# Kernel tuning notes

Hardware: AMD Instinct MI355X
Metric: run time of the kernel (lower is better)

The kernel has to match this reference:

```python
import jax, jax.numpy as jnp
import numpy as np

N, D, F, K = 50000, 256, 256, 10


def setup_inputs() -> dict:
    key = jax.random.key(0)
    k1, k2, k3, k4, k5, k6 = jax.random.split(key, 6)
    # neighbor indices in [-1, N); -1 marks padding (masked out in forward)
    return {
        "Z1": jax.random.normal(k1, (N, D), dtype=jnp.float32),
        "Z2": jax.random.normal(k2, (N, D), dtype=jnp.float32),
        "Wr": jax.random.normal(k3, (D, F), dtype=jnp.float32),
        "Wnr": jax.random.normal(k4, (D, F), dtype=jnp.float32),
        "n1": jax.random.randint(k5, (N, K), -1, N, dtype=jnp.int64),
        "n2": jax.random.randint(k6, (N, K), -1, N, dtype=jnp.int64),
    }


def _protein(Z, nb, Wr, Wnr):
    residues_signal = Z @ Wr                      # [N, F]
    neighbors_base_signal = Z @ Wnr               # [N, F]
    mask = (nb > -1)                              # [N, K]
    # index -1 wraps to last row (as in torch), then is zeroed by the mask
    feats = neighbors_base_signal[nb] * mask[..., None].astype(Z.dtype)  # [N, K, F]
    norm = jnp.maximum(mask.sum(axis=1), 1).astype(Z.dtype)[:, None]     # [N, 1]
    neighbors_signal = feats.sum(axis=1) / norm
    return jax.nn.relu(residues_signal + neighbors_signal)


def reference(Z1, Z2, Wr, Wnr, n1, n2):
    out1 = _protein(Z1, n1, Wr, Wnr)
    out2 = _protein(Z2, n2, Wr, Wnr)
    return jnp.stack([out1, out2])  # [2, N, F]
```

## Files before the change

kernel.cpp:

```cpp
#include <hip/hip_runtime.h>
#include <hip/hip_bf16.h>
#include <hip/hip_fp8.h>

#define NNODE 50000
#define MTOT  100000
#define NF    256
#define KNB   10

typedef unsigned short u16;
typedef float f32x4 __attribute__((ext_vector_type(4)));
typedef float f32x2 __attribute__((ext_vector_type(2)));
typedef short bf16x8 __attribute__((ext_vector_type(8)));

__device__ __forceinline__ u16 f2bf(float f) {
    unsigned u = __builtin_bit_cast(unsigned, f);
    unsigned r = (u + 0x7fffu + ((u >> 16) & 1u)) >> 16;
    return (u16)r;
}
__device__ __forceinline__ unsigned char f2f8(float f) {
    return (unsigned char)__hip_fp8_e4m3(f).__x;
}
__device__ __forceinline__ float f8tof(unsigned char b) {
    __hip_fp8_e4m3 h;
    h.__x = (__hip_fp8_storage_t)b;
    return (float)h;
}
template <int WORD>
__device__ __forceinline__ f32x2 cvt2_fp8(unsigned v) {
#if __has_builtin(__builtin_amdgcn_cvt_pk_f32_fp8)
    auto c = __builtin_amdgcn_cvt_pk_f32_fp8((int)v, WORD);
    f32x2 r; r.x = c[0]; r.y = c[1];
    return r;
#else
    unsigned s = WORD ? (v >> 16) : v;
    f32x2 r;
    r.x = f8tof((unsigned char)(s & 0xff));
    r.y = f8tof((unsigned char)((s >> 8) & 0xff));
    return r;
#endif
}
template <int WORD>
__device__ __forceinline__ unsigned pk_fp8(float a, float b, unsigned old) {
#if __has_builtin(__builtin_amdgcn_cvt_pk_fp8_f32)
    return (unsigned)__builtin_amdgcn_cvt_pk_fp8_f32(a, b, (int)old, WORD);
#else
    unsigned lo = (unsigned)f2f8(a) | ((unsigned)f2f8(b) << 8);
    return WORD ? ((old & 0x0000ffffu) | (lo << 16)) : ((old & 0xffff0000u) | lo);
#endif
}
__device__ __forceinline__ void gload_lds16(const void* g, void* l) {
    __builtin_amdgcn_global_load_lds(
        (const __attribute__((address_space(1))) unsigned int*)g,
        (__attribute__((address_space(3))) unsigned int*)l, 16, 0, 0);
}

__global__ __launch_bounds__(256) void cast_all(const float* __restrict__ Z1,
                                                const float* __restrict__ Z2,
                                                const float* __restrict__ Wr,
                                                const float* __restrict__ Wnr,
                                                u16* __restrict__ Zleft,
                                                unsigned char* __restrict__ Z8,
                                                u16* __restrict__ WT,
                                                unsigned char* __restrict__ WT8) {
    int b = blockIdx.x;
    if (b < 12500) {
        unsigned id = b * 256 + threadIdx.x;
        int m = id >> 5;
        int d = (id & 31) << 3;
        const float* src = (m < NNODE) ? (Z1 + (size_t)m * 256 + d)
                                       : (Z2 + (size_t)(m - NNODE) * 256 + d);
        float4 a = *(const float4*)src;
        float4 bb = *(const float4*)(src + 4);
        uint4 o;
        o.x = (unsigned)f2bf(a.x) | ((unsigned)f2bf(a.y) << 16);
        o.y = (unsigned)f2bf(a.z) | ((unsigned)f2bf(a.w) << 16);
        o.z = (unsigned)f2bf(bb.x) | ((unsigned)f2bf(bb.y) << 16);
        o.w = (unsigned)f2bf(bb.z) | ((unsigned)f2bf(bb.w) << 16);
        *(uint4*)(Zleft + (size_t)m * 256 + d) = o;
        uint2 o8;
        o8.x = (unsigned)f2f8(a.x) | ((unsigned)f2f8(a.y) << 8) |
               ((unsigned)f2f8(a.z) << 16) | ((unsigned)f2f8(a.w) << 24);
        o8.y = (unsigned)f2f8(bb.x) | ((unsigned)f2f8(bb.y) << 8) |
               ((unsigned)f2f8(bb.z) << 16) | ((unsigned)f2f8(bb.w) << 24);
        *(uint2*)(Z8 + (size_t)m * 256 + d) = o8;
    } else if (b < 12756) {
        int id = (b - 12500) * 256 + threadIdx.x;
        int n = id >> 8, k = id & 255;
        WT[n * 256 + k] = f2bf(Wr[(size_t)k * 256 + n]);
    } else {
        int id = (b - 12756) * 256 + threadIdx.x;
        int n = id >> 8, k = id & 255;
        WT8[n * 256 + k] = f2f8(Wnr[(size_t)k * 256 + n]);
    }
}

__device__ __forceinline__ void stageA(const u16* __restrict__ A, u16* dst,
                                       int m0, int kt, int t) {
    int row = t >> 2, gd = t & 3;
    int gs = gd ^ (row & 3);
    int grow = m0 + row;
    if (grow >= MTOT) grow = MTOT - 1;
    gload_lds16(A + (size_t)grow * 256 + kt + gs * 8, dst + t * 8);
}
__device__ __forceinline__ void stageBl(const u16* __restrict__ WT, u16* dst,
                                        int kt, int t) {
    #pragma unroll
    for (int rp = 0; rp < 2; ++rp) {
        int c = rp * 512 + t;
        int col = c >> 2, gd = c & 3;
        int gs = gd ^ (col & 3);
        gload_lds16(WT + (size_t)col * 256 + kt + gs * 8, dst + c * 8);
    }
}
__device__ __forceinline__ void stageBr(const unsigned char* __restrict__ WT8,
                                        unsigned char* dst, int ktr, int t) {
    #pragma unroll
    for (int rp = 0; rp < 2; ++rp) {
        int c = rp * 512 + t;
        int col = c >> 2, gd = c & 3;
        int gs = gd ^ (col & 3);
        gload_lds16(WT8 + (size_t)col * 256 + ktr + gs * 16, dst + c * 16);
    }
}

__device__ __forceinline__ void mfma_left(const u16* sAc, const u16* sBc, int lane,
                                          int wr, int wc, f32x4 (&acc)[4][4]) {
    const int hi = lane >> 4, l15 = lane & 15;
    bf16x8 af[4], bfr[4];
    #pragma unroll
    for (int i = 0; i < 4; ++i) {
        int row = wr * 64 + i * 16 + l15;
        af[i] = *(const bf16x8*)&sAc[row * 32 + ((hi ^ (row & 3)) << 3)];
    }
    #pragma unroll
    for (int j = 0; j < 4; ++j) {
        int col = wc * 64 + j * 16 + l15;
        bfr[j] = *(const bf16x8*)&sBc[col * 32 + ((hi ^ (col & 3)) << 3)];
    }
    #pragma unroll
    for (int i = 0; i < 4; ++i)
        #pragma unroll
        for (int j = 0; j < 4; ++j)
            acc[i][j] = __builtin_amdgcn_mfma_f32_16x16x32_bf16(af[i], bfr[j], acc[i][j], 0, 0, 0);
}
__device__ __forceinline__ void mfma_right(const unsigned char* sZc, const unsigned char* sBc,
                                           int ktr, int lane, int wr, int wc,
                                           f32x4 (&acc)[4][4]) {
    const int hi = lane >> 4, l15 = lane & 15;
    #pragma unroll
    for (int kk = 0; kk < 64; kk += 32) {
        long long az[4], bz[4];
        #pragma unroll
        for (int i = 0; i < 4; ++i) {
            int row = wr * 64 + i * 16 + l15;
            int gr = ((ktr + kk) >> 3) + hi;
            az[i] = *(const long long*)&sZc[row * 256 + ((gr ^ (row & 7)) << 3)];
        }
        #pragma unroll
        for (int j = 0; j < 4; ++j) {
            int col = wc * 64 + j * 16 + l15;
            int kb = kk + hi * 8;
            bz[j] = *(const long long*)&sBc[col * 64 + (((kb >> 4) ^ (col & 3)) << 4) + (kb & 15)];
        }
        #pragma unroll
        for (int i = 0; i < 4; ++i)
            #pragma unroll
            for (int j = 0; j < 4; ++j)
                acc[i][j] = __builtin_amdgcn_mfma_f32_16x16x32_fp8_fp8(az[i], bz[j], acc[i][j], 0, 0, 0);
    }
}

template <int S>
__device__ __forceinline__ void left_step(const u16* __restrict__ Zl,
                                          const u16* __restrict__ WT,
                                          const unsigned char* __restrict__ WT8,
                                          const unsigned char* __restrict__ Z8,
                                          const int* __restrict__ n1,
                                          const int* __restrict__ n2,
                                          u16* sA0, u16* sA1, u16* sB0, u16* sB1,
                                          unsigned char* sZ,
                                          int m0, int t, int lane, int w, int wr, int wc,
                                          f32x4 (&acc)[4][4]) {
    u16* sAcur = (S & 1) ? sA1 : sA0;
    u16* sAnxt = (S & 1) ? sA0 : sA1;
    u16* sBcur = (S & 1) ? sB1 : sB0;
    u16* sBnxt = (S & 1) ? sB0 : sB1;
    int rl = (w << 4) + (S << 1) + (lane >> 5);
    int g = m0 + rl;
    if (g >= MTOT) g = MTOT - 1;
    int p = (g >= NNODE);
    const int* nb = (p ? n2 : n1) + (size_t)(g - p * NNODE) * KNB;
    int idxa[KNB];
    #pragma unroll
    for (int q = 0; q < 5; ++q) {
        int2 v = *(const int2*)(nb + 2 * q);
        idxa[2 * q] = v.x;
        idxa[2 * q + 1] = v.y;
    }
    const unsigned char* zb = Z8 + (size_t)p * ((size_t)NNODE * 256) + ((lane & 31) << 3);
    uint2 gv[KNB];
    #pragma unroll
    for (int k = 0; k < KNB; ++k)
        gv[k] = *(const uint2*)(zb + (size_t)(idxa[k] > -1 ? idxa[k] : 0) * 256);
    if (S < 7) {
        stageA(Zl, sAnxt, m0, (S + 1) * 32, t);
        stageBl(WT, sBnxt, (S + 1) * 32, t);
    } else {
        stageBr(WT8, (unsigned char*)sBnxt, 0, t);
    }
    f32x2 a0 = {0.f, 0.f}, a1 = {0.f, 0.f}, a2 = {0.f, 0.f}, a3 = {0.f, 0.f};
    int cnt = 0;
    #pragma unroll
    for (int k = 0; k < KNB; ++k) {
        int valid = (idxa[k] > -1) ? 1 : 0;
        cnt += valid;
        float mm = (float)valid;
        f32x2 m2 = {mm, mm};
        uint2 v = gv[k];
        a0 += m2 * cvt2_fp8<0>(v.x);
        a1 += m2 * cvt2_fp8<1>(v.x);
        a2 += m2 * cvt2_fp8<0>(v.y);
        a3 += m2 * cvt2_fp8<1>(v.y);
    }
    float sc = 1.0f / (float)(cnt > 0 ? cnt : 1);
    unsigned w0 = pk_fp8<0>(a0.x * sc, a0.y * sc, 0u);
    w0 = pk_fp8<1>(a1.x * sc, a1.y * sc, w0);
    unsigned w1 = pk_fp8<0>(a2.x * sc, a2.y * sc, 0u);
    w1 = pk_fp8<1>(a3.x * sc, a3.y * sc, w1);
    int gp = (lane & 31) ^ (rl & 7);
    *(uint2*)(sZ + rl * 256 + (gp << 3)) = make_uint2(w0, w1);
    if (S == 7) asm volatile("s_waitcnt lgkmcnt(0)" ::: "memory");
    __builtin_amdgcn_s_barrier();
    __builtin_amdgcn_s_setprio(1);
    mfma_left(sAcur, sBcur, lane, wr, wc, acc);
    __builtin_amdgcn_s_setprio(0);
    __builtin_amdgcn_s_barrier();
}

template <int R>
__device__ __forceinline__ void right_step(const unsigned char* __restrict__ WT8,
                                           u16* sB0, u16* sB1, unsigned char* sZ,
                                           int t, int lane, int wr, int wc,
                                           f32x4 (&acc)[4][4]) {
    unsigned char* sBcur = (unsigned char*)((R & 1) ? sB1 : sB0);
    unsigned char* sBnxt = (unsigned char*)((R & 1) ? sB0 : sB1);
    if (R < 3) {
        stageBr(WT8, sBnxt, (R + 1) * 64, t);
        asm volatile("s_waitcnt vmcnt(2)" ::: "memory");
    } else {
        asm volatile("s_waitcnt vmcnt(0)" ::: "memory");
    }
    __builtin_amdgcn_s_barrier();
    __builtin_amdgcn_s_setprio(1);
    mfma_right(sZ, sBcur, R * 64, lane, wr, wc, acc);
    __builtin_amdgcn_s_setprio(0);
    if (R < 3) __builtin_amdgcn_s_barrier();
}

__global__ __launch_bounds__(512, 4) void gemm_fused(const u16* __restrict__ Zl,
                                                     const unsigned char* __restrict__ Z8,
                                                     const u16* __restrict__ WT,
                                                     const unsigned char* __restrict__ WT8,
                                                     const int* __restrict__ n1,
                                                     const int* __restrict__ n2,
                                                     float* __restrict__ C) {
    __shared__ u16 sA[2][128 * 32];
    __shared__ u16 sB[2][256 * 32];
    __shared__ unsigned char sZ[128 * 256];
    const int m0 = blockIdx.x * 128;
    const int t = threadIdx.x;
    const int lane = t & 63;
    const int w = t >> 6;
    const int wr = w >> 2, wc = w & 3;

    f32x4 acc[4][4] = {};

    stageA(Zl, &sA[0][0], m0, 0, t);
    stageBl(WT, &sB[0][0], 0, t);

    left_step<0>(Zl, WT, WT8, Z8, n1, n2, &sA[0][0], &sA[1][0], &sB[0][0], &sB[1][0], sZ, m0, t, lane, w, wr, wc, acc);
    left_step<1>(Zl, WT, WT8, Z8, n1, n2, &sA[0][0], &sA[1][0], &sB[0][0], &sB[1][0], sZ, m0, t, lane, w, wr, wc, acc);
    left_step<2>(Zl, WT, WT8, Z8, n1, n2, &sA[0][0], &sA[1][0], &sB[0][0], &sB[1][0], sZ, m0, t, lane, w, wr, wc, acc);
    left_step<3>(Zl, WT, WT8, Z8, n1, n2, &sA[0][0], &sA[1][0], &sB[0][0], &sB[1][0], sZ, m0, t, lane, w, wr, wc, acc);
    left_step<4>(Zl, WT, WT8, Z8, n1, n2, &sA[0][0], &sA[1][0], &sB[0][0], &sB[1][0], sZ, m0, t, lane, w, wr, wc, acc);
    left_step<5>(Zl, WT, WT8, Z8, n1, n2, &sA[0][0], &sA[1][0], &sB[0][0], &sB[1][0], sZ, m0, t, lane, w, wr, wc, acc);
    left_step<6>(Zl, WT, WT8, Z8, n1, n2, &sA[0][0], &sA[1][0], &sB[0][0], &sB[1][0], sZ, m0, t, lane, w, wr, wc, acc);
    left_step<7>(Zl, WT, WT8, Z8, n1, n2, &sA[0][0], &sA[1][0], &sB[0][0], &sB[1][0], sZ, m0, t, lane, w, wr, wc, acc);

    right_step<0>(WT8, &sB[0][0], &sB[1][0], sZ, t, lane, wr, wc, acc);
    right_step<1>(WT8, &sB[0][0], &sB[1][0], sZ, t, lane, wr, wc, acc);
    right_step<2>(WT8, &sB[0][0], &sB[1][0], sZ, t, lane, wr, wc, acc);
    right_step<3>(WT8, &sB[0][0], &sB[1][0], sZ, t, lane, wr, wc, acc);

    const int l15 = lane & 15;
    #pragma unroll
    for (int i = 0; i < 4; ++i) {
        int rbase = m0 + wr * 64 + i * 16 + ((lane >> 4) << 2);
        #pragma unroll
        for (int j = 0; j < 4; ++j) {
            int col = wc * 64 + j * 16 + l15;
            #pragma unroll
            for (int q = 0; q < 4; ++q) {
                int row = rbase + q;
                if (row < MTOT) C[(size_t)row * NF + col] = fmaxf(acc[i][j][q], 0.f);
            }
        }
    }
}

extern "C" void kernel_launch(void* const* d_in, const int* in_sizes, int n_in,
                              void* d_out, int out_size, void* d_ws, size_t ws_size,
                              hipStream_t stream) {
    const float* Z1  = (const float*)d_in[0];
    const float* Z2  = (const float*)d_in[1];
    const float* Wr  = (const float*)d_in[2];
    const float* Wnr = (const float*)d_in[3];
    const int*   n1  = (const int*)d_in[4];
    const int*   n2  = (const int*)d_in[5];
    float* out = (float*)d_out;

    u16* WT            = (u16*)d_ws;
    unsigned char* WT8 = (unsigned char*)d_ws + 131072;
    u16* Zleft         = (u16*)((unsigned char*)d_ws + 196608);
    unsigned char* Z8  = (unsigned char*)d_ws + 196608 + (size_t)MTOT * 512;

    cast_all<<<13012, 256, 0, stream>>>(Z1, Z2, Wr, Wnr, Zleft, Z8, WT, WT8);
    gemm_fused<<<782, 512, 0, stream>>>(Zleft, Z8, WT, WT8, n1, n2, out);
}
```

Baseline: 135.9 us.

## Halve M tile, widen K step, software-pipeline neighbor gathers across steps

The fused GEMM tile drops from 128 to 64 rows, so the grid grows to 1563 blocks, and the left GEMM K step widens from 32 to 64 with 8-way swizzling. Neighbor index loads and fp8 gathers are now software-pipelined: indices for the next step and gathers for the current step are issued while the previous step's gathered rows are averaged into shared memory. Shared memory is reorganised into one aliased 64KB buffer, and the fp8 weight layout gets an extra XOR swizzle to avoid LDS bank conflicts. Smaller tiles mean more weight reloads per output row, in exchange for more blocks and better latency hiding of the gathers.

```diff
diff --git a/kernel.cpp b/kernel.cpp
--- a/kernel.cpp
+++ b/kernel.cpp
@@ -90,25 +90,26 @@
     } else {
         int id = (b - 12756) * 256 + threadIdx.x;
         int n = id >> 8, k = id & 255;
-        WT8[n * 256 + k] = f2f8(Wnr[(size_t)k * 256 + n]);
-    }
-}
-
-__device__ __forceinline__ void stageA(const u16* __restrict__ A, u16* dst,
+        int kb = k ^ (((n >> 2) & 1) << 3);
+        WT8[n * 256 + kb] = f2f8(Wnr[(size_t)k * 256 + n]);
+    }
+}
+
+__device__ __forceinline__ void stageA(const u16* __restrict__ Zl, u16* dst,
                                        int m0, int kt, int t) {
-    int row = t >> 2, gd = t & 3;
-    int gs = gd ^ (row & 3);
+    int row = t >> 3, gd = t & 7;
+    int gs = gd ^ (row & 7);
     int grow = m0 + row;
     if (grow >= MTOT) grow = MTOT - 1;
-    gload_lds16(A + (size_t)grow * 256 + kt + gs * 8, dst + t * 8);
+    gload_lds16(Zl + (size_t)grow * 256 + kt + gs * 8, dst + t * 8);
 }
 __device__ __forceinline__ void stageBl(const u16* __restrict__ WT, u16* dst,
                                         int kt, int t) {
     #pragma unroll
-    for (int rp = 0; rp < 2; ++rp) {
+    for (int rp = 0; rp < 4; ++rp) {
         int c = rp * 512 + t;
-        int col = c >> 2, gd = c & 3;
-        int gs = gd ^ (col & 3);
+        int col = c >> 3, gd = c & 7;
+        int gs = gd ^ (col & 7);
         gload_lds16(WT + (size_t)col * 256 + kt + gs * 8, dst + c * 8);
     }
 }
@@ -124,137 +125,139 @@
 }
 
 __device__ __forceinline__ void mfma_left(const u16* sAc, const u16* sBc, int lane,
-                                          int wr, int wc, f32x4 (&acc)[4][4]) {
+                                          int wr, int wc, f32x4 (&acc)[2][4]) {
     const int hi = lane >> 4, l15 = lane & 15;
-    bf16x8 af[4], bfr[4];
-    #pragma unroll
-    for (int i = 0; i < 4; ++i) {
-        int row = wr * 64 + i * 16 + l15;
-        af[i] = *(const bf16x8*)&sAc[row * 32 + ((hi ^ (row & 3)) << 3)];
-    }
-    #pragma unroll
-    for (int j = 0; j < 4; ++j) {
-        int col = wc * 64 + j * 16 + l15;
-        bfr[j] = *(const bf16x8*)&sBc[col * 32 + ((hi ^ (col & 3)) << 3)];
-    }
-    #pragma unroll
-    for (int i = 0; i < 4; ++i)
-        #pragma unroll
-        for (int j = 0; j < 4; ++j)
-            acc[i][j] = __builtin_amdgcn_mfma_f32_16x16x32_bf16(af[i], bfr[j], acc[i][j], 0, 0, 0);
-}
-__device__ __forceinline__ void mfma_right(const unsigned char* sZc, const unsigned char* sBc,
-                                           int ktr, int lane, int wr, int wc,
-                                           f32x4 (&acc)[4][4]) {
-    const int hi = lane >> 4, l15 = lane & 15;
     #pragma unroll
     for (int kk = 0; kk < 64; kk += 32) {
-        long long az[4], bz[4];
-        #pragma unroll
-        for (int i = 0; i < 4; ++i) {
-            int row = wr * 64 + i * 16 + l15;
-            int gr = ((ktr + kk) >> 3) + hi;
-            az[i] = *(const long long*)&sZc[row * 256 + ((gr ^ (row & 7)) << 3)];
+        int g = (kk >> 3) + hi;
+        bf16x8 af[2], bfr[4];
+        #pragma unroll
+        for (int i = 0; i < 2; ++i) {
+            int row = wr * 32 + i * 16 + l15;
+            af[i] = *(const bf16x8*)((const char*)sAc + row * 128 + ((g ^ (row & 7)) << 4));
         }
         #pragma unroll
         for (int j = 0; j < 4; ++j) {
             int col = wc * 64 + j * 16 + l15;
-            int kb = kk + hi * 8;
-            bz[j] = *(const long long*)&sBc[col * 64 + (((kb >> 4) ^ (col & 3)) << 4) + (kb & 15)];
-        }
-        #pragma unroll
-        for (int i = 0; i < 4; ++i)
+            bfr[j] = *(const bf16x8*)((const char*)sBc + col * 128 + ((g ^ (col & 7)) << 4));
+        }
+        #pragma unroll
+        for (int i = 0; i < 2; ++i)
+            #pragma unroll
+            for (int j = 0; j < 4; ++j)
+                acc[i][j] = __builtin_amdgcn_mfma_f32_16x16x32_bf16(af[i], bfr[j], acc[i][j], 0, 0, 0);
+    }
+}
+__device__ __forceinline__ void mfma_right(const unsigned char* sZ, const unsigned char* sBc,
+                                           int R, int lane, int wr, int wc,
+                                           f32x4 (&acc)[2][4]) {
+    const int hi = lane >> 4, l15 = lane & 15;
+    #pragma unroll
+    for (int m = 0; m < 2; ++m) {
+        long long az[2], bz[4];
+        #pragma unroll
+        for (int i = 0; i < 2; ++i) {
+            int row = wr * 32 + i * 16 + l15;
+            int g8 = R * 8 + m * 4 + hi;
+            az[i] = *(const long long*)(sZ + row * 256 + ((g8 ^ (row & 7)) << 3));
+        }
+        #pragma unroll
+        for (int j = 0; j < 4; ++j) {
+            int col = wc * 64 + j * 16 + l15;
+            int G = 2 * m + (hi >> 1);
+            int hb = ((hi & 1) ^ ((col >> 2) & 1)) << 3;
+            bz[j] = *(const long long*)(sBc + col * 64 + ((G ^ (col & 3)) << 4) + hb);
+        }
+        #pragma unroll
+        for (int i = 0; i < 2; ++i)
             #pragma unroll
             for (int j = 0; j < 4; ++j)
                 acc[i][j] = __builtin_amdgcn_mfma_f32_16x16x32_fp8_fp8(az[i], bz[j], acc[i][j], 0, 0, 0);
     }
 }
 
-template <int S>
-__device__ __forceinline__ void left_step(const u16* __restrict__ Zl,
-                                          const u16* __restrict__ WT,
-                                          const unsigned char* __restrict__ WT8,
-                                          const unsigned char* __restrict__ Z8,
-                                          const int* __restrict__ n1,
-                                          const int* __restrict__ n2,
-                                          u16* sA0, u16* sA1, u16* sB0, u16* sB1,
-                                          unsigned char* sZ,
-                                          int m0, int t, int lane, int w, int wr, int wc,
-                                          f32x4 (&acc)[4][4]) {
-    u16* sAcur = (S & 1) ? sA1 : sA0;
-    u16* sAnxt = (S & 1) ? sA0 : sA1;
-    u16* sBcur = (S & 1) ? sB1 : sB0;
-    u16* sBnxt = (S & 1) ? sB0 : sB1;
-    int rl = (w << 4) + (S << 1) + (lane >> 5);
-    int g = m0 + rl;
-    if (g >= MTOT) g = MTOT - 1;
-    int p = (g >= NNODE);
-    const int* nb = (p ? n2 : n1) + (size_t)(g - p * NNODE) * KNB;
-    int idxa[KNB];
-    #pragma unroll
-    for (int q = 0; q < 5; ++q) {
-        int2 v = *(const int2*)(nb + 2 * q);
-        idxa[2 * q] = v.x;
-        idxa[2 * q + 1] = v.y;
-    }
-    const unsigned char* zb = Z8 + (size_t)p * ((size_t)NNODE * 256) + ((lane & 31) << 3);
-    uint2 gv[KNB];
-    #pragma unroll
-    for (int k = 0; k < KNB; ++k)
-        gv[k] = *(const uint2*)(zb + (size_t)(idxa[k] > -1 ? idxa[k] : 0) * 256);
-    if (S < 7) {
-        stageA(Zl, sAnxt, m0, (S + 1) * 32, t);
-        stageBl(WT, sBnxt, (S + 1) * 32, t);
-    } else {
-        stageBr(WT8, (unsigned char*)sBnxt, 0, t);
-    }
+__device__ __forceinline__ void consume(const uint2 (&gv)[KNB], unsigned mask, int cnt,
+                                        int w, int lane, int s, unsigned char* sZ) {
     f32x2 a0 = {0.f, 0.f}, a1 = {0.f, 0.f}, a2 = {0.f, 0.f}, a3 = {0.f, 0.f};
-    int cnt = 0;
     #pragma unroll
     for (int k = 0; k < KNB; ++k) {
-        int valid = (idxa[k] > -1) ? 1 : 0;
-        cnt += valid;
-        float mm = (float)valid;
+        float mm = (float)((mask >> k) & 1u);
         f32x2 m2 = {mm, mm};
-        uint2 v = gv[k];
-        a0 += m2 * cvt2_fp8<0>(v.x);
-        a1 += m2 * cvt2_fp8<1>(v.x);
-        a2 += m2 * cvt2_fp8<0>(v.y);
-        a3 += m2 * cvt2_fp8<1>(v.y);
+        a0 += m2 * cvt2_fp8<0>(gv[k].x);
+        a1 += m2 * cvt2_fp8<1>(gv[k].x);
+        a2 += m2 * cvt2_fp8<0>(gv[k].y);
+        a3 += m2 * cvt2_fp8<1>(gv[k].y);
     }
     float sc = 1.0f / (float)(cnt > 0 ? cnt : 1);
     unsigned w0 = pk_fp8<0>(a0.x * sc, a0.y * sc, 0u);
     w0 = pk_fp8<1>(a1.x * sc, a1.y * sc, w0);
     unsigned w1 = pk_fp8<0>(a2.x * sc, a2.y * sc, 0u);
     w1 = pk_fp8<1>(a3.x * sc, a3.y * sc, w1);
+    int rl = w * 8 + s * 2 + (lane >> 5);
     int gp = (lane & 31) ^ (rl & 7);
     *(uint2*)(sZ + rl * 256 + (gp << 3)) = make_uint2(w0, w1);
-    if (S == 7) asm volatile("s_waitcnt lgkmcnt(0)" ::: "memory");
+}
+
+template <int S>
+__device__ __forceinline__ void left_step(const u16* __restrict__ Zl,
+                                          const u16* __restrict__ WT,
+                                          const unsigned char* __restrict__ Z8,
+                                          const int* __restrict__ n1,
+                                          const int* __restrict__ n2,
+                                          u16* sA0, u16* sA1, u16* sBL, unsigned char* sZ,
+                                          int m0, int t, int lane, int w, int wr, int wc,
+                                          int2 (&icur)[5], unsigned& pmask, int& pcnt,
+                                          uint2 (&gv)[KNB], f32x4 (&acc)[2][4]) {
+    u16* sAcur = (S & 1) ? sA1 : sA0;
+    u16* sAnxt = (S & 1) ? sA0 : sA1;
+    stageBl(WT, sBL, S * 64, t);
+    __builtin_amdgcn_sched_barrier(0);
+    if (S < 3) stageA(Zl, sAnxt, m0, (S + 1) * 64, t);
+    __builtin_amdgcn_sched_barrier(0);
+    int2 inxt[5];
+    if (S < 3) {
+        int rl = w * 8 + (S + 1) * 2 + (lane >> 5);
+        int g = m0 + rl;
+        if (g >= MTOT) g = MTOT - 1;
+        int p = (g >= NNODE);
+        const int* nb = (p ? n2 : n1) + (size_t)(g - p * NNODE) * KNB;
+        #pragma unroll
+        for (int q = 0; q < 5; ++q) inxt[q] = *(const int2*)(nb + 2 * q);
+    }
+    __builtin_amdgcn_sched_barrier(0);
+    if (S > 0) consume(gv, pmask, pcnt, w, lane, S - 1, sZ);
+    __builtin_amdgcn_sched_barrier(0);
+    {
+        int rl = w * 8 + S * 2 + (lane >> 5);
+        int g = m0 + rl;
+        if (g >= MTOT) g = MTOT - 1;
+        int p = (g >= NNODE);
+        const unsigned char* zb = Z8 + (size_t)p * ((size_t)NNODE * 256) + ((lane & 31) << 3);
+        unsigned mask = 0;
+        int cnt = 0;
+        #pragma unroll
+        for (int k = 0; k < KNB; ++k) {
+            int ix = (k & 1) ? icur[k >> 1].y : icur[k >> 1].x;
+            int valid = (ix > -1) ? 1 : 0;
+            mask |= (unsigned)valid << k;
+            cnt += valid;
+            gv[k] = *(const uint2*)(zb + (size_t)(valid ? ix : 0) * 256);
+        }
+        pmask = mask;
+        pcnt = cnt;
+    }
+    if (S < 3) {
+        #pragma unroll
+        for (int q = 0; q < 5; ++q) icur[q] = inxt[q];
+    }
+    __builtin_amdgcn_sched_barrier(0);
+    if (S < 3) asm volatile("s_waitcnt vmcnt(16)" ::: "memory");
+    else       asm volatile("s_waitcnt vmcnt(10)" ::: "memory");
     __builtin_amdgcn_s_barrier();
     __builtin_amdgcn_s_setprio(1);
-    mfma_left(sAcur, sBcur, lane, wr, wc, acc);
+    mfma_left(sAcur, sBL, lane, wr, wc, acc);
     __builtin_amdgcn_s_setprio(0);
     __builtin_amdgcn_s_barrier();
-}
-
-template <int R>
-__device__ __forceinline__ void right_step(const unsigned char* __restrict__ WT8,
-                                           u16* sB0, u16* sB1, unsigned char* sZ,
-                                           int t, int lane, int wr, int wc,
-                                           f32x4 (&acc)[4][4]) {
-    unsigned char* sBcur = (unsigned char*)((R & 1) ? sB1 : sB0);
-    unsigned char* sBnxt = (unsigned char*)((R & 1) ? sB0 : sB1);
-    if (R < 3) {
-        stageBr(WT8, sBnxt, (R + 1) * 64, t);
-        asm volatile("s_waitcnt vmcnt(2)" ::: "memory");
-    } else {
-        asm volatile("s_waitcnt vmcnt(0)" ::: "memory");
-    }
-    __builtin_amdgcn_s_barrier();
-    __builtin_amdgcn_s_setprio(1);
-    mfma_right(sZ, sBcur, R * 64, lane, wr, wc, acc);
-    __builtin_amdgcn_s_setprio(0);
-    if (R < 3) __builtin_amdgcn_s_barrier();
 }
 
 __global__ __launch_bounds__(512, 4) void gemm_fused(const u16* __restrict__ Zl,
@@ -264,38 +267,73 @@
                                                      const int* __restrict__ n1,
                                                      const int* __restrict__ n2,
                                                      float* __restrict__ C) {
-    __shared__ u16 sA[2][128 * 32];
-    __shared__ u16 sB[2][256 * 32];
-    __shared__ unsigned char sZ[128 * 256];
-    const int m0 = blockIdx.x * 128;
+    __shared__ char smem[65536];
+    u16* sA0 = (u16*)smem;
+    u16* sA1 = (u16*)(smem + 8192);
+    u16* sBL = (u16*)(smem + 16384);
+    unsigned char* sBr0 = (unsigned char*)(smem + 16384);
+    unsigned char* sBr1 = (unsigned char*)(smem + 32768);
+    unsigned char* sZ = (unsigned char*)(smem + 49152);
+
+    const int m0 = blockIdx.x * 64;
     const int t = threadIdx.x;
     const int lane = t & 63;
     const int w = t >> 6;
     const int wr = w >> 2, wc = w & 3;
 
-    f32x4 acc[4][4] = {};
-
-    stageA(Zl, &sA[0][0], m0, 0, t);
-    stageBl(WT, &sB[0][0], 0, t);
-
-    left_step<0>(Zl, WT, WT8, Z8, n1, n2, &sA[0][0], &sA[1][0], &sB[0][0], &sB[1][0], sZ, m0, t, lane, w, wr, wc, acc);
-    left_step<1>(Zl, WT, WT8, Z8, n1, n2, &sA[0][0], &sA[1][0], &sB[0][0], &sB[1][0], sZ, m0, t, lane, w, wr, wc, acc);
-    left_step<2>(Zl, WT, WT8, Z8, n1, n2, &sA[0][0], &sA[1][0], &sB[0][0], &sB[1][0], sZ, m0, t, lane, w, wr, wc, acc);
-    left_step<3>(Zl, WT, WT8, Z8, n1, n2, &sA[0][0], &sA[1][0], &sB[0][0], &sB[1][0], sZ, m0, t, lane, w, wr, wc, acc);
-    left_step<4>(Zl, WT, WT8, Z8, n1, n2, &sA[0][0], &sA[1][0], &sB[0][0], &sB[1][0], sZ, m0, t, lane, w, wr, wc, acc);
-    left_step<5>(Zl, WT, WT8, Z8, n1, n2, &sA[0][0], &sA[1][0], &sB[0][0], &sB[1][0], sZ, m0, t, lane, w, wr, wc, acc);
-    left_step<6>(Zl, WT, WT8, Z8, n1, n2, &sA[0][0], &sA[1][0], &sB[0][0], &sB[1][0], sZ, m0, t, lane, w, wr, wc, acc);
-    left_step<7>(Zl, WT, WT8, Z8, n1, n2, &sA[0][0], &sA[1][0], &sB[0][0], &sB[1][0], sZ, m0, t, lane, w, wr, wc, acc);
-
-    right_step<0>(WT8, &sB[0][0], &sB[1][0], sZ, t, lane, wr, wc, acc);
-    right_step<1>(WT8, &sB[0][0], &sB[1][0], sZ, t, lane, wr, wc, acc);
-    right_step<2>(WT8, &sB[0][0], &sB[1][0], sZ, t, lane, wr, wc, acc);
-    right_step<3>(WT8, &sB[0][0], &sB[1][0], sZ, t, lane, wr, wc, acc);
+    f32x4 acc[2][4] = {};
+    uint2 gv[KNB];
+    int2 icur[5];
+    unsigned pmask = 0;
+    int pcnt = 0;
+
+    stageA(Zl, sA0, m0, 0, t);
+    {
+        int rl = w * 8 + (lane >> 5);
+        int g = m0 + rl;
+        if (g >= MTOT) g = MTOT - 1;
+        int p = (g >= NNODE);
+        const int* nb = (p ? n2 : n1) + (size_t)(g - p * NNODE) * KNB;
+        #pragma unroll
+        for (int q = 0; q < 5; ++q) icur[q] = *(const int2*)(nb + 2 * q);
+    }
+
+    left_step<0>(Zl, WT, Z8, n1, n2, sA0, sA1, sBL, sZ, m0, t, lane, w, wr, wc, icur, pmask, pcnt, gv, acc);
+    left_step<1>(Zl, WT, Z8, n1, n2, sA0, sA1, sBL, sZ, m0, t, lane, w, wr, wc, icur, pmask, pcnt, gv, acc);
+    left_step<2>(Zl, WT, Z8, n1, n2, sA0, sA1, sBL, sZ, m0, t, lane, w, wr, wc, icur, pmask, pcnt, gv, acc);
+    left_step<3>(Zl, WT, Z8, n1, n2, sA0, sA1, sBL, sZ, m0, t, lane, w, wr, wc, icur, pmask, pcnt, gv, acc);
+
+    consume(gv, pmask, pcnt, w, lane, 3, sZ);
+    stageBr(WT8, sBr0, 0, t);
+    asm volatile("s_waitcnt vmcnt(0)" ::: "memory");
+    asm volatile("s_waitcnt lgkmcnt(0)" ::: "memory");
+    __builtin_amdgcn_s_barrier();
+
+#define RSTEP(R)                                                            \
+    do {                                                                    \
+        if ((R) < 3) {                                                      \
+            stageBr(WT8, ((R) & 1) ? sBr0 : sBr1, ((R) + 1) * 64, t);       \
+            asm volatile("s_waitcnt vmcnt(2)" ::: "memory");                \
+        } else {                                                            \
+            asm volatile("s_waitcnt vmcnt(0)" ::: "memory");                \
+        }                                                                   \
+        __builtin_amdgcn_s_barrier();                                       \
+        __builtin_amdgcn_s_setprio(1);                                      \
+        mfma_right(sZ, ((R) & 1) ? sBr1 : sBr0, (R), lane, wr, wc, acc);    \
+        __builtin_amdgcn_s_setprio(0);                                      \
+        if ((R) < 3) __builtin_amdgcn_s_barrier();                          \
+    } while (0)
+
+    RSTEP(0);
+    RSTEP(1);
+    RSTEP(2);
+    RSTEP(3);
+#undef RSTEP
 
     const int l15 = lane & 15;
     #pragma unroll
-    for (int i = 0; i < 4; ++i) {
-        int rbase = m0 + wr * 64 + i * 16 + ((lane >> 4) << 2);
+    for (int i = 0; i < 2; ++i) {
+        int rbase = m0 + wr * 32 + i * 16 + ((lane >> 4) << 2);
         #pragma unroll
         for (int j = 0; j < 4; ++j) {
             int col = wc * 64 + j * 16 + l15;
@@ -325,5 +363,5 @@
     unsigned char* Z8  = (unsigned char*)d_ws + 196608 + (size_t)MTOT * 512;
 
     cast_all<<<13012, 256, 0, stream>>>(Z1, Z2, Wr, Wnr, Zleft, Z8, WT, WT8);
-    gemm_fused<<<782, 512, 0, stream>>>(Zleft, Z8, WT, WT8, n1, n2, out);
-}
+    gemm_fused<<<1563, 512, 0, stream>>>(Zleft, Z8, WT, WT8, n1, n2, out);
+}
```

Result: faster. 110.6 us (-18.6%).
